# Performance work log

Hardware: AMD Instinct MI355X
Metric: run time of the kernel (lower is better)

## Reference

```python
import jax, jax.numpy as jnp
import numpy as np

TOP_K = 8


def setup_inputs() -> dict:
    key = jax.random.key(0)
    ks = jax.random.split(key, 8)
    B, S, H, BD, N, VBD = 4, 2048, 2048, 256, 256, 256
    return {
        "hidden_states": jax.random.normal(ks[0], (B, S, H), jnp.float32),
        "primary_attention_output": jax.random.normal(ks[1], (B, S, H), jnp.float32),
        "q_proj_w": jax.random.normal(ks[2], (BD, H), jnp.float32) / np.sqrt(H),
        "slot_keys": jax.random.normal(ks[3], (N, BD), jnp.float32),
        "slot_values": jax.random.normal(ks[4], (N, H), jnp.float32),
        "reliability": jax.random.uniform(ks[5], (N,), jnp.float32, 1e-3, 1.0),
        "value_down_w": jax.random.normal(ks[6], (VBD, H), jnp.float32) * 0.1 / np.sqrt(H),
        "value_up_w": jax.random.normal(ks[7], (H, VBD), jnp.float32) * 0.1 / np.sqrt(VBD),
    }


def reference(hidden_states, primary_attention_output, q_proj_w, slot_keys,
              slot_values, reliability, value_down_w, value_up_w):
    B, S, H = hidden_states.shape
    BD = q_proj_w.shape[0]
    # query = q_proj(hidden_states): [B,S,BD]
    query = jnp.einsum("bsh,dh->bsd", hidden_states, q_proj_w)
    # gate-chain scoring: query . slot_keys scaled, plus log-reliability mask
    rel_mask = jnp.log(jnp.clip(reliability, 1e-10))            # [N]
    scores = jnp.einsum("bsd,nd->bsn", query, slot_keys) / jnp.sqrt(
        jnp.asarray(BD, query.dtype)) + rel_mask                # [B,S,N]
    top_scores, top_idx = jax.lax.top_k(scores, TOP_K)          # [B,S,K]
    attn = jax.nn.softmax(top_scores, axis=-1)                  # [B,S,K]
    final_gate = jax.nn.sigmoid(top_scores[..., 0])             # [B,S]
    # slot-pool gather + weighted sum of values (irregular access)
    vals = slot_values[top_idx]                                 # [B,S,K,H]
    aux = jnp.einsum("bsk,bskh->bsh", attn, vals)               # [B,S,H]
    # low-rank value projection with GELU
    aux = jnp.einsum("bsh,vh->bsv", aux, value_down_w)
    aux = jax.nn.gelu(aux)
    aux = jnp.einsum("bsv,hv->bsh", aux, value_up_w)
    return primary_attention_output + final_gate[..., None] * aux
```

## Files before the change

kernel.cpp:

```cpp
#include <hip/hip_runtime.h>
#include <stdint.h>


typedef float f32x4 __attribute__((ext_vector_type(4)));
typedef unsigned short u16x8 __attribute__((ext_vector_type(8)));
typedef unsigned short u16x4 __attribute__((ext_vector_type(4)));
typedef __bf16 bf16x8 __attribute__((ext_vector_type(8)));

#define WS_QW    0u
#define WS_SK    1048576u
#define WS_SV    1179648u
#define WS_VDW   2228224u
#define WS_VUP   3276800u
#define WS_REL   4325376u
#define WS_PV    4326400u
#define WS_GATE  4588544u
#define WS_QP    4621312u
#define WS_D     21398528u

static __device__ __forceinline__ unsigned short f2bf(float f) {
  union { float f; unsigned int u; } v; v.f = f;
  unsigned int r = v.u + 0x7FFFu + ((v.u >> 16) & 1u);
  return (unsigned short)(r >> 16);
}
static __device__ __forceinline__ bf16x8 as_bf16(u16x8 v) {
  return __builtin_bit_cast(bf16x8, v);
}
static __device__ __forceinline__ float gelu_tanh(float x) {
  float u = 0.7978845608028654f * (x + 0.044715f * x * x * x);
  return 0.5f * x * (1.0f + tanhf(u));
}

__global__ void k_prep(const float* __restrict__ qw, const float* __restrict__ sk,
                       const float* __restrict__ sv, const float* __restrict__ vdw,
                       const float* __restrict__ vup, const float* __restrict__ rel,
                       unsigned char* __restrict__ ws) {
  unsigned short* o_qw  = (unsigned short*)(ws + WS_QW);
  unsigned short* o_sk  = (unsigned short*)(ws + WS_SK);
  unsigned short* o_sv  = (unsigned short*)(ws + WS_SV);
  unsigned short* o_vdw = (unsigned short*)(ws + WS_VDW);
  unsigned short* o_vup = (unsigned short*)(ws + WS_VUP);
  float* o_rel = (float*)(ws + WS_REL);
  int tid = blockIdx.x * blockDim.x + threadIdx.x;
  int stride = gridDim.x * blockDim.x;
  for (int g = tid; g < 540736; g += stride) {
    const float* src; unsigned short* dst; int i;
    if      (g < 131072) { src = qw;  dst = o_qw;  i = g; }
    else if (g < 147456) { src = sk;  dst = o_sk;  i = g - 131072; }
    else if (g < 278528) { src = sv;  dst = o_sv;  i = g - 147456; }
    else if (g < 409600) { src = vdw; dst = o_vdw; i = g - 278528; }
    else if (g < 540672) { src = vup; dst = o_vup; i = g - 409600; }
    else {
      int i4 = (g - 540672) * 4;
      #pragma unroll
      for (int j = 0; j < 4; j++) o_rel[i4 + j] = logf(fmaxf(rel[i4 + j], 1e-10f));
      continue;
    }
    f32x4 v = *(const f32x4*)(src + (size_t)i * 4);
    u16x4 o;
    #pragma unroll
    for (int j = 0; j < 4; j++) o[j] = f2bf(v[j]);
    *(u16x4*)(dst + (size_t)i * 4) = o;
  }
}

__global__ __launch_bounds__(256, 4) void k_pv(unsigned char* __restrict__ ws) {
  const unsigned short* sv  = (const unsigned short*)(ws + WS_SV);
  const unsigned short* vdw = (const unsigned short*)(ws + WS_VDW);
  float* PV = (float*)(ws + WS_PV);
  __shared__ float red[4][16][16];
  int t = threadIdx.x, lane = t & 63, w = t >> 6;
  int nt = blockIdx.x >> 4, vt = blockIdx.x & 15;
  const unsigned short* aLane = sv  + (size_t)(nt * 16 + (lane & 15)) * 2048 + (lane >> 4) * 8 + w * 512;
  const unsigned short* bLane = vdw + (size_t)(vt * 16 + (lane & 15)) * 2048 + (lane >> 4) * 8 + w * 512;
  f32x4 acc = {0.f, 0.f, 0.f, 0.f};
  #pragma unroll
  for (int kt = 0; kt < 16; kt++) {
    bf16x8 a = as_bf16(*(const u16x8*)(aLane + kt * 32));
    bf16x8 b = as_bf16(*(const u16x8*)(bLane + kt * 32));
    acc = __builtin_amdgcn_mfma_f32_16x16x32_bf16(a, b, acc, 0, 0, 0);
  }
  int col = lane & 15, row0 = (lane >> 4) * 4;
  #pragma unroll
  for (int j = 0; j < 4; j++) red[w][row0 + j][col] = acc[j];
  __syncthreads();
  if (w == 0) {
    #pragma unroll
    for (int i = 0; i < 4; i++) {
      int idx = i * 64 + lane, r = idx >> 4, c = idx & 15;
      float s = red[0][r][c] + red[1][r][c] + red[2][r][c] + red[3][r][c];
      PV[(nt * 16 + r) * 256 + vt * 16 + c] = s;
    }
  }
}

__global__ __launch_bounds__(256, 4) void k_query(const float* __restrict__ hs,
                                                  unsigned char* __restrict__ ws) {
  const unsigned short* qw = (const unsigned short*)(ws + WS_QW);
  float* qp = (float*)(ws + WS_QP);
  __shared__ __align__(16) unsigned short As[32 * 64];
  __shared__ __align__(16) unsigned short Bs[256 * 64];
  int t = threadIdx.x, lane = t & 63, w = t >> 6;
  int rt = blockIdx.x >> 1, ks = blockIdx.x & 1;
  int row0 = rt * 32, kbase = ks * 1024;
  f32x4 acc[2][4] = {};
  int sr = t >> 3, sc = t & 7;
  const float* aptr = hs + (size_t)(row0 + sr) * 2048 + kbase + sc * 8;
  const unsigned short* bptr = qw + (size_t)sr * 2048 + kbase + sc * 8;
  f32x4 pa0, pa1;
  u16x8 pb0, pb1, pb2, pb3, pb4, pb5, pb6, pb7;
  pa0 = *(const f32x4*)(aptr);
  pa1 = *(const f32x4*)(aptr + 4);
  pb0 = *(const u16x8*)(bptr + (size_t)0 * 32 * 2048);
  pb1 = *(const u16x8*)(bptr + (size_t)1 * 32 * 2048);
  pb2 = *(const u16x8*)(bptr + (size_t)2 * 32 * 2048);
  pb3 = *(const u16x8*)(bptr + (size_t)3 * 32 * 2048);
  pb4 = *(const u16x8*)(bptr + (size_t)4 * 32 * 2048);
  pb5 = *(const u16x8*)(bptr + (size_t)5 * 32 * 2048);
  pb6 = *(const u16x8*)(bptr + (size_t)6 * 32 * 2048);
  pb7 = *(const u16x8*)(bptr + (size_t)7 * 32 * 2048);
  for (int kt = 0; kt < 16; kt++) {
    __syncthreads();
    {
      u16x8 o;
      #pragma unroll
      for (int j = 0; j < 4; j++) { o[j] = f2bf(pa0[j]); o[4 + j] = f2bf(pa1[j]); }
      *(u16x8*)&As[sr * 64 + ((sc ^ (sr & 7)) * 8)] = o;
      u16x8 pb[8] = {pb0, pb1, pb2, pb3, pb4, pb5, pb6, pb7};
      #pragma unroll
      for (int i = 0; i < 8; i++) {
        int n = i * 32 + sr;
        *(u16x8*)&Bs[n * 64 + ((sc ^ (n & 7)) * 8)] = pb[i];
      }
    }
    __syncthreads();
    if (kt < 15) {
      int off = (kt + 1) * 64;
      pa0 = *(const f32x4*)(aptr + off);
      pa1 = *(const f32x4*)(aptr + off + 4);
      pb0 = *(const u16x8*)(bptr + (size_t)0 * 32 * 2048 + off);
      pb1 = *(const u16x8*)(bptr + (size_t)1 * 32 * 2048 + off);
      pb2 = *(const u16x8*)(bptr + (size_t)2 * 32 * 2048 + off);
      pb3 = *(const u16x8*)(bptr + (size_t)3 * 32 * 2048 + off);
      pb4 = *(const u16x8*)(bptr + (size_t)4 * 32 * 2048 + off);
      pb5 = *(const u16x8*)(bptr + (size_t)5 * 32 * 2048 + off);
      pb6 = *(const u16x8*)(bptr + (size_t)6 * 32 * 2048 + off);
      pb7 = *(const u16x8*)(bptr + (size_t)7 * 32 * 2048 + off);
    }
    #pragma unroll
    for (int kk = 0; kk < 2; kk++) {
      int ck = kk * 4 + (lane >> 4);
      bf16x8 a[2], b[4];
      #pragma unroll
      for (int mf = 0; mf < 2; mf++) {
        int arow = mf * 16 + (lane & 15);
        a[mf] = as_bf16(*(const u16x8*)&As[arow * 64 + ((ck ^ (arow & 7)) * 8)]);
      }
      #pragma unroll
      for (int nf = 0; nf < 4; nf++) {
        int brow = w * 64 + nf * 16 + (lane & 15);
        b[nf] = as_bf16(*(const u16x8*)&Bs[brow * 64 + ((ck ^ (brow & 7)) * 8)]);
      }
      #pragma unroll
      for (int mf = 0; mf < 2; mf++)
        #pragma unroll
        for (int nf = 0; nf < 4; nf++)
          acc[mf][nf] = __builtin_amdgcn_mfma_f32_16x16x32_bf16(a[mf], b[nf], acc[mf][nf], 0, 0, 0);
    }
  }
  float* outp = qp + (size_t)ks * 8192 * 256;
  #pragma unroll
  for (int mf = 0; mf < 2; mf++) {
    int row = row0 + mf * 16 + (lane >> 4) * 4;
    #pragma unroll
    for (int nf = 0; nf < 4; nf++) {
      int col = w * 64 + nf * 16 + (lane & 15);
      #pragma unroll
      for (int j = 0; j < 4; j++) outp[(size_t)(row + j) * 256 + col] = acc[mf][nf][j];
    }
  }
}

#define QSTR 264
#define SSTR 260
__global__ __launch_bounds__(256, 4) void k_score(unsigned char* __restrict__ ws) {
  const float* qp = (const float*)(ws + WS_QP);
  const unsigned short* sk = (const unsigned short*)(ws + WS_SK);
  const float* relm = (const float*)(ws + WS_REL);
  const float* PV = (const float*)(ws + WS_PV);
  float* gates = (float*)(ws + WS_GATE);
  unsigned short* D = (unsigned short*)(ws + WS_D);
  __shared__ __align__(16) unsigned short Qs[16 * QSTR];
  __shared__ __align__(16) float Ss[16 * SSTR];
  int t = threadIdx.x, lane = t & 63, w = t >> 6;
  int row0 = blockIdx.x * 16;
  #pragma unroll
  for (int i = 0; i < 4; i++) {
    int id = i * 256 + t, r = id >> 6, c4 = id & 63;
    const float* p0 = qp + (size_t)(row0 + r) * 256 + c4 * 4;
    f32x4 a = *(const f32x4*)p0;
    f32x4 b = *(const f32x4*)(p0 + 8192 * 256);
    u16x4 o;
    #pragma unroll
    for (int j = 0; j < 4; j++) o[j] = f2bf(a[j] + b[j]);
    *(u16x4*)&Qs[r * QSTR + c4 * 4] = o;
  }
  __syncthreads();
  {
    f32x4 acc[4] = {};
    for (int ksb = 0; ksb < 8; ksb++) {
      int ck = lane >> 4;
      bf16x8 a = as_bf16(*(const u16x8*)&Qs[(lane & 15) * QSTR + ksb * 32 + ck * 8]);
      #pragma unroll
      for (int nf = 0; nf < 4; nf++) {
        int n = w * 64 + nf * 16 + (lane & 15);
        bf16x8 b = as_bf16(*(const u16x8*)&sk[(size_t)n * 256 + ksb * 32 + ck * 8]);
        acc[nf] = __builtin_amdgcn_mfma_f32_16x16x32_bf16(a, b, acc[nf], 0, 0, 0);
      }
    }
    #pragma unroll
    for (int nf = 0; nf < 4; nf++) {
      int n = w * 64 + nf * 16 + (lane & 15);
      float rm = relm[n];
      int rr = (lane >> 4) * 4;
      #pragma unroll
      for (int j = 0; j < 4; j++) Ss[(rr + j) * SSTR + n] = acc[nf][j] * 0.0625f + rm;
    }
  }
  __syncthreads();
  for (int rr = 0; rr < 4; rr++) {
    int row = w * 4 + rr;
    f32x4 sv4 = *(const f32x4*)&Ss[row * SSTR + lane * 4];
    unsigned int key[4];
    #pragma unroll
    for (int j = 0; j < 4; j++) {
      unsigned int u = __builtin_bit_cast(unsigned int, sv4[j]);
      unsigned int os = (u & 0x80000000u) ? ~u : (u | 0x80000000u);
      key[j] = (os & 0xFFFFFF00u) | (unsigned int)(255 - (lane * 4 + j));
    }
    unsigned int win[8];
    #pragma unroll
    for (int e = 0; e < 8; e++) {
      unsigned int m01 = key[0] > key[1] ? key[0] : key[1];
      unsigned int m23 = key[2] > key[3] ? key[2] : key[3];
      unsigned int m = m01 > m23 ? m01 : m23;
      #pragma unroll
      for (int d = 1; d < 64; d <<= 1) {
        unsigned int o = (unsigned int)__shfl_xor((int)m, d, 64);
        m = o > m ? o : m;
      }
      win[e] = m;
      #pragma unroll
      for (int j = 0; j < 4; j++) if (key[j] == m) key[j] = 0u;
    }
    float s8[8]; int i8[8];
    #pragma unroll
    for (int e = 0; e < 8; e++) {
      i8[e] = 255 - (int)(win[e] & 0xFFu);
      unsigned int os = win[e] & 0xFFFFFF00u;
      unsigned int u = (os & 0x80000000u) ? (os ^ 0x80000000u) : ~os;
      s8[e] = __builtin_bit_cast(float, u);
    }
    float m0 = s8[0], sum = 0.f, we[8];
    #pragma unroll
    for (int e = 0; e < 8; e++) { we[e] = expf(s8[e] - m0); sum += we[e]; }
    float inv = 1.f / sum;
    f32x4 accv = {0.f, 0.f, 0.f, 0.f};
    #pragma unroll
    for (int e = 0; e < 8; e++) {
      float wk = we[e] * inv;
      f32x4 p = *(const f32x4*)(PV + (size_t)i8[e] * 256 + lane * 4);
      #pragma unroll
      for (int j = 0; j < 4; j++) accv[j] += wk * p[j];
    }
    u16x4 o;
    #pragma unroll
    for (int j = 0; j < 4; j++) o[j] = f2bf(gelu_tanh(accv[j]));
    *(u16x4*)&D[(size_t)(row0 + row) * 256 + lane * 4] = o;
    if (lane == 0) gates[row0 + row] = 1.f / (1.f + expf(-m0));
  }
}

union KOutLds {
  unsigned short AB[12288];
  float stage[32 * 132];
};
__global__ __launch_bounds__(256, 4) void k_out(const float* __restrict__ primary,
                                                float* __restrict__ out,
                                                unsigned char* __restrict__ ws) {
  const unsigned short* D = (const unsigned short*)(ws + WS_D);
  const unsigned short* vup = (const unsigned short*)(ws + WS_VUP);
  const float* gates = (const float*)(ws + WS_GATE);
  __shared__ __align__(16) KOutLds u;
  __shared__ float gate_s[64];
  unsigned short* As = u.AB;
  unsigned short* Bs = u.AB + 4096;
  int t = threadIdx.x, lane = t & 63, w = t >> 6;
  int bid = blockIdx.x;
  int L = (bid & 7) * 256 + (bid >> 3);
  int rt = L >> 4, ct = L & 15;
  int wm = w >> 1, wn = w & 1;
  const float* pbase = primary + (size_t)(rt * 64 + (t >> 5)) * 2048 + ct * 128 + (t & 31) * 4;
  f32x4 pref[2][4];
  #pragma unroll
  for (int i = 0; i < 4; i++)
    pref[0][i] = *(const f32x4*)(pbase + (size_t)(i * 8) * 2048);
  int sr = t >> 3, sc = t & 7;
  const unsigned short* aptr = D + (size_t)(rt * 64 + sr) * 256 + sc * 8;
  const unsigned short* bptr = vup + (size_t)(ct * 128 + sr) * 256 + sc * 8;
  u16x8 pA0, pA1, pB0, pB1, pB2, pB3;
  pA0 = *(const u16x8*)(aptr);
  pA1 = *(const u16x8*)(aptr + 32 * 256);
  pB0 = *(const u16x8*)(bptr);
  pB1 = *(const u16x8*)(bptr + 32 * 256);
  pB2 = *(const u16x8*)(bptr + 64 * 256);
  pB3 = *(const u16x8*)(bptr + 96 * 256);
  if (t < 64) gate_s[t] = gates[rt * 64 + t];
  f32x4 acc[2][4] = {};
  for (int k0 = 0; k0 < 256; k0 += 64) {
    __syncthreads();
    {
      int r0 = sr, r1 = sr + 32, r2 = sr + 64, r3 = sr + 96;
      *(u16x8*)&As[r0 * 64 + ((sc ^ (r0 & 7)) * 8)] = pA0;
      *(u16x8*)&As[r1 * 64 + ((sc ^ (r1 & 7)) * 8)] = pA1;
      *(u16x8*)&Bs[r0 * 64 + ((sc ^ (r0 & 7)) * 8)] = pB0;
      *(u16x8*)&Bs[r1 * 64 + ((sc ^ (r1 & 7)) * 8)] = pB1;
      *(u16x8*)&Bs[r2 * 64 + ((sc ^ (r2 & 7)) * 8)] = pB2;
      *(u16x8*)&Bs[r3 * 64 + ((sc ^ (r3 & 7)) * 8)] = pB3;
    }
    __syncthreads();
    if (k0 < 192) {
      int off = k0 + 64;
      pA0 = *(const u16x8*)(aptr + off);
      pA1 = *(const u16x8*)(aptr + 32 * 256 + off);
      pB0 = *(const u16x8*)(bptr + off);
      pB1 = *(const u16x8*)(bptr + 32 * 256 + off);
      pB2 = *(const u16x8*)(bptr + 64 * 256 + off);
      pB3 = *(const u16x8*)(bptr + 96 * 256 + off);
    }
    #pragma unroll
    for (int kk = 0; kk < 2; kk++) {
      int ck = kk * 4 + (lane >> 4);
      bf16x8 a[2], b[4];
      #pragma unroll
      for (int mf = 0; mf < 2; mf++) {
        int ar = wm * 32 + mf * 16 + (lane & 15);
        a[mf] = as_bf16(*(const u16x8*)&As[ar * 64 + ((ck ^ (ar & 7)) * 8)]);
      }
      #pragma unroll
      for (int nf = 0; nf < 4; nf++) {
        int br = wn * 64 + nf * 16 + (lane & 15);
        b[nf] = as_bf16(*(const u16x8*)&Bs[br * 64 + ((ck ^ (br & 7)) * 8)]);
      }
      #pragma unroll
      for (int mf = 0; mf < 2; mf++)
        #pragma unroll
        for (int nf = 0; nf < 4; nf++)
          acc[mf][nf] = __builtin_amdgcn_mfma_f32_16x16x32_bf16(a[mf], b[nf], acc[mf][nf], 0, 0, 0);
    }
  }
  #pragma unroll
  for (int c = 0; c < 2; c++) {
    __syncthreads();
    if (wm == c) {
      #pragma unroll
      for (int mf = 0; mf < 2; mf++) {
        #pragma unroll
        for (int nf = 0; nf < 4; nf++) {
          int col = wn * 64 + nf * 16 + (lane & 15);
          #pragma unroll
          for (int j = 0; j < 4; j++) {
            int r = mf * 16 + (lane >> 4) * 4 + j;
            u.stage[r * 132 + col] = acc[mf][nf][j];
          }
        }
      }
    }
    if (c == 0) {
      #pragma unroll
      for (int i = 0; i < 4; i++)
        pref[1][i] = *(const f32x4*)(pbase + (size_t)(32 + i * 8) * 2048);
    }
    __syncthreads();
    #pragma unroll
    for (int i = 0; i < 4; i++) {
      int idx = i * 256 + t, r = idx >> 5, c4 = idx & 31;
      int row = rt * 64 + c * 32 + r;
      size_t o = (size_t)row * 2048 + ct * 128 + c4 * 4;
      f32x4 p = pref[c][i];
      f32x4 s = *(const f32x4*)&u.stage[r * 132 + c4 * 4];
      float g = gate_s[c * 32 + r];
      f32x4 ov;
      #pragma unroll
      for (int j = 0; j < 4; j++) ov[j] = p[j] + g * s[j];
      *(f32x4*)(out + o) = ov;
    }
  }
}

extern "C" void kernel_launch(void* const* d_in, const int* in_sizes, int n_in,
                              void* d_out, int out_size, void* d_ws, size_t ws_size,
                              hipStream_t stream) {
  const float* hs      = (const float*)d_in[0];
  const float* primary = (const float*)d_in[1];
  const float* qw      = (const float*)d_in[2];
  const float* sk      = (const float*)d_in[3];
  const float* sv      = (const float*)d_in[4];
  const float* rel     = (const float*)d_in[5];
  const float* vdw     = (const float*)d_in[6];
  const float* vup     = (const float*)d_in[7];
  unsigned char* ws = (unsigned char*)d_ws;
  float* out = (float*)d_out;

  k_prep<<<dim3(256), dim3(256), 0, stream>>>(qw, sk, sv, vdw, vup, rel, ws);
  k_pv<<<dim3(256), dim3(256), 0, stream>>>(ws);
  k_query<<<dim3(512), dim3(256), 0, stream>>>(hs, ws);
  k_score<<<dim3(512), dim3(256), 0, stream>>>(ws);
  k_out<<<dim3(2048), dim3(256), 0, stream>>>(primary, out, ws);
}
```

Baseline: 83.79 us.

## Load MFMA operands directly from global memory in k_out, dropping LDS staging

The output GEMM no longer stages the D and value_up tiles through shared memory with double-buffered register prefetch and barriers. Each wave now loads its bf16 MFMA fragments straight from global/L2 and runs a fully unrolled K loop. This removes the LDS writes, the swizzled reads and two barriers per K step, and shrinks the shared footprint. In exchange, operands shared across waves are fetched redundantly from cache, and the per-lane 16-byte loads are strided across rows, which may coalesce poorly.

Result: slower. 109.4 us (+30.5%).

```diff
diff --git a/kernel.cpp b/kernel.cpp
--- a/kernel.cpp
+++ b/kernel.cpp
@@ -281,20 +281,14 @@
   }
 }
 
-union KOutLds {
-  unsigned short AB[12288];
-  float stage[32 * 132];
-};
 __global__ __launch_bounds__(256, 4) void k_out(const float* __restrict__ primary,
                                                 float* __restrict__ out,
                                                 unsigned char* __restrict__ ws) {
   const unsigned short* D = (const unsigned short*)(ws + WS_D);
   const unsigned short* vup = (const unsigned short*)(ws + WS_VUP);
   const float* gates = (const float*)(ws + WS_GATE);
-  __shared__ __align__(16) KOutLds u;
+  __shared__ __align__(16) float stage[32 * 132];
   __shared__ float gate_s[64];
-  unsigned short* As = u.AB;
-  unsigned short* Bs = u.AB + 4096;
   int t = threadIdx.x, lane = t & 63, w = t >> 6;
   int bid = blockIdx.x;
   int L = (bid & 7) * 256 + (bid >> 3);
@@ -305,59 +299,31 @@
   #pragma unroll
   for (int i = 0; i < 4; i++)
     pref[0][i] = *(const f32x4*)(pbase + (size_t)(i * 8) * 2048);
-  int sr = t >> 3, sc = t & 7;
-  const unsigned short* aptr = D + (size_t)(rt * 64 + sr) * 256 + sc * 8;
-  const unsigned short* bptr = vup + (size_t)(ct * 128 + sr) * 256 + sc * 8;
-  u16x8 pA0, pA1, pB0, pB1, pB2, pB3;
-  pA0 = *(const u16x8*)(aptr);
-  pA1 = *(const u16x8*)(aptr + 32 * 256);
-  pB0 = *(const u16x8*)(bptr);
-  pB1 = *(const u16x8*)(bptr + 32 * 256);
-  pB2 = *(const u16x8*)(bptr + 64 * 256);
-  pB3 = *(const u16x8*)(bptr + 96 * 256);
   if (t < 64) gate_s[t] = gates[rt * 64 + t];
+  const unsigned short* aB0 = D + (size_t)(rt * 64 + wm * 32 + (lane & 15)) * 256 + (lane >> 4) * 8;
+  const unsigned short* aB1 = aB0 + 16 * 256;
+  const unsigned short* bB0 = vup + (size_t)(ct * 128 + wn * 64 + (lane & 15)) * 256 + (lane >> 4) * 8;
+  const unsigned short* bB1 = bB0 + 16 * 256;
+  const unsigned short* bB2 = bB0 + 32 * 256;
+  const unsigned short* bB3 = bB0 + 48 * 256;
   f32x4 acc[2][4] = {};
-  for (int k0 = 0; k0 < 256; k0 += 64) {
-    __syncthreads();
-    {
-      int r0 = sr, r1 = sr + 32, r2 = sr + 64, r3 = sr + 96;
-      *(u16x8*)&As[r0 * 64 + ((sc ^ (r0 & 7)) * 8)] = pA0;
-      *(u16x8*)&As[r1 * 64 + ((sc ^ (r1 & 7)) * 8)] = pA1;
-      *(u16x8*)&Bs[r0 * 64 + ((sc ^ (r0 & 7)) * 8)] = pB0;
-      *(u16x8*)&Bs[r1 * 64 + ((sc ^ (r1 & 7)) * 8)] = pB1;
-      *(u16x8*)&Bs[r2 * 64 + ((sc ^ (r2 & 7)) * 8)] = pB2;
-      *(u16x8*)&Bs[r3 * 64 + ((sc ^ (r3 & 7)) * 8)] = pB3;
-    }
-    __syncthreads();
-    if (k0 < 192) {
-      int off = k0 + 64;
-      pA0 = *(const u16x8*)(aptr + off);
-      pA1 = *(const u16x8*)(aptr + 32 * 256 + off);
-      pB0 = *(const u16x8*)(bptr + off);
-      pB1 = *(const u16x8*)(bptr + 32 * 256 + off);
-      pB2 = *(const u16x8*)(bptr + 64 * 256 + off);
-      pB3 = *(const u16x8*)(bptr + 96 * 256 + off);
-    }
-    #pragma unroll
-    for (int kk = 0; kk < 2; kk++) {
-      int ck = kk * 4 + (lane >> 4);
-      bf16x8 a[2], b[4];
-      #pragma unroll
-      for (int mf = 0; mf < 2; mf++) {
-        int ar = wm * 32 + mf * 16 + (lane & 15);
-        a[mf] = as_bf16(*(const u16x8*)&As[ar * 64 + ((ck ^ (ar & 7)) * 8)]);
-      }
-      #pragma unroll
-      for (int nf = 0; nf < 4; nf++) {
-        int br = wn * 64 + nf * 16 + (lane & 15);
-        b[nf] = as_bf16(*(const u16x8*)&Bs[br * 64 + ((ck ^ (br & 7)) * 8)]);
-      }
-      #pragma unroll
-      for (int mf = 0; mf < 2; mf++)
-        #pragma unroll
-        for (int nf = 0; nf < 4; nf++)
-          acc[mf][nf] = __builtin_amdgcn_mfma_f32_16x16x32_bf16(a[mf], b[nf], acc[mf][nf], 0, 0, 0);
-    }
+  #pragma unroll
+  for (int kt = 0; kt < 8; kt++) {
+    int off = kt * 32;
+    bf16x8 a0 = as_bf16(*(const u16x8*)(aB0 + off));
+    bf16x8 a1 = as_bf16(*(const u16x8*)(aB1 + off));
+    bf16x8 b0 = as_bf16(*(const u16x8*)(bB0 + off));
+    bf16x8 b1 = as_bf16(*(const u16x8*)(bB1 + off));
+    bf16x8 b2 = as_bf16(*(const u16x8*)(bB2 + off));
+    bf16x8 b3 = as_bf16(*(const u16x8*)(bB3 + off));
+    acc[0][0] = __builtin_amdgcn_mfma_f32_16x16x32_bf16(a0, b0, acc[0][0], 0, 0, 0);
+    acc[0][1] = __builtin_amdgcn_mfma_f32_16x16x32_bf16(a0, b1, acc[0][1], 0, 0, 0);
+    acc[0][2] = __builtin_amdgcn_mfma_f32_16x16x32_bf16(a0, b2, acc[0][2], 0, 0, 0);
+    acc[0][3] = __builtin_amdgcn_mfma_f32_16x16x32_bf16(a0, b3, acc[0][3], 0, 0, 0);
+    acc[1][0] = __builtin_amdgcn_mfma_f32_16x16x32_bf16(a1, b0, acc[1][0], 0, 0, 0);
+    acc[1][1] = __builtin_amdgcn_mfma_f32_16x16x32_bf16(a1, b1, acc[1][1], 0, 0, 0);
+    acc[1][2] = __builtin_amdgcn_mfma_f32_16x16x32_bf16(a1, b2, acc[1][2], 0, 0, 0);
+    acc[1][3] = __builtin_amdgcn_mfma_f32_16x16x32_bf16(a1, b3, acc[1][3], 0, 0, 0);
   }
   #pragma unroll
   for (int c = 0; c < 2; c++) {
@@ -371,7 +337,7 @@
           #pragma unroll
           for (int j = 0; j < 4; j++) {
             int r = mf * 16 + (lane >> 4) * 4 + j;
-            u.stage[r * 132 + col] = acc[mf][nf][j];
+            stage[r * 132 + col] = acc[mf][nf][j];
           }
         }
       }
@@ -388,7 +354,7 @@
       int row = rt * 64 + c * 32 + r;
       size_t o = (size_t)row * 2048 + ct * 128 + c4 * 4;
       f32x4 p = pref[c][i];
-      f32x4 s = *(const f32x4*)&u.stage[r * 132 + c4 * 4];
+      f32x4 s = *(const f32x4*)&stage[r * 132 + c4 * 4];
       float g = gate_s[c * 32 + r];
       f32x4 ov;
       #pragma unroll
```
